# Kernel optimization log

Hardware: AMD Instinct MI355X
Metric: run time of the kernel (lower is better)

Reference implementation:

```python
import jax, jax.numpy as jnp
import numpy as np

B, N, HID = 2, 512, 768
BIAF = 256
CLS = 14
CH = 32
SIZE_DIM = 25
N_POS = 30
HSZ = 2 * (BIAF + 1) + SIZE_DIM


def setup_inputs() -> dict:
    key = jax.random.key(0)
    ks = jax.random.split(key, 16)
    s = 0.02
    return {
        "x": jax.random.normal(ks[0], (B, N, HID), jnp.float32),
        "y": jax.random.normal(ks[1], (B, N, HID), jnp.float32),
        "z": jax.random.normal(ks[2], (B, N, N, CH), jnp.float32),
        "mlp1_w": jax.random.normal(ks[3], (BIAF, HID), jnp.float32) * s,
        "mlp1_b": jnp.zeros((BIAF,), jnp.float32),
        "mlp2_w": jax.random.normal(ks[4], (BIAF, HID), jnp.float32) * s,
        "mlp2_b": jnp.zeros((BIAF,), jnp.float32),
        "head_w": jax.random.normal(ks[5], (BIAF, HID), jnp.float32) * s,
        "head_b": jnp.zeros((BIAF,), jnp.float32),
        "tail_w": jax.random.normal(ks[6], (BIAF, HID), jnp.float32) * s,
        "tail_b": jnp.zeros((BIAF,), jnp.float32),
        "biaf_W": jax.random.normal(ks[7], (CLS, BIAF + 1, BIAF + 1), jnp.float32) * s,
        "W": jax.random.normal(ks[8], (CLS, HSZ), jnp.float32) * s,
        "size_emb": jax.random.normal(ks[9], (N_POS, SIZE_DIM), jnp.float32) * s,
    }


def reference(x, y, z, mlp1_w, mlp1_b, mlp2_w, mlp2_b, head_w, head_b,
              tail_w, tail_b, biaf_W, W, size_emb):
    # MLP branches (dropout=0 at eval; torch GELU is exact erf)
    h = jax.nn.gelu(x @ mlp1_w.T + mlp1_b, approximate=False)   # (b,m,BIAF)
    t = jax.nn.gelu(y @ mlp2_w.T + mlp2_b, approximate=False)   # (b,n,BIAF)
    ones = jnp.ones(h.shape[:-1] + (1,), h.dtype)
    h1 = jnp.concatenate([h, ones], -1)                          # (b,m,BIAF+1)
    t1 = jnp.concatenate([t, ones], -1)                          # (b,n,BIAF+1)
    # Biaffine with bias_x=bias_y=True -> (b,cls,m,n)
    o1 = jnp.einsum('bmi,kij,bnj->bkmn', h1, biaf_W, t1)

    # head/tail MLPs with LeakyReLU(0.01), then append 1-column
    head = jax.nn.leaky_relu(x @ head_w.T + head_b, 0.01)
    tail = jax.nn.leaky_relu(x @ tail_w.T + tail_b, 0.01)
    head = jnp.concatenate([head, ones], -1)                     # (b,m,BIAF+1)
    tail = jnp.concatenate([tail, ones], -1)                     # (b,n,BIAF+1)

    # einsum('bmnh,kh->bkmn', cat([head_m, tail_n, size_mn]), W) decomposed so
    # the (b,m,n,HSZ) pairwise tensor is never materialized (same math).
    d = head.shape[-1]
    Wh, Wt, Ws = W[:, :d], W[:, d:2 * d], W[:, 2 * d:]
    n = x.shape[1]
    ar = jnp.arange(n)
    ids = jnp.clip(ar[None, :] - ar[:, None], -N_POS // 2, N_POS // 2 - 1) + N_POS // 2
    se = size_emb[ids]                                           # (m,n,SIZE_DIM)
    o3 = (jnp.einsum('bmh,kh->bkm', head, Wh)[:, :, :, None]
          + jnp.einsum('bnh,kh->bkn', tail, Wt)[:, :, None, :]
          + jnp.einsum('mnh,kh->kmn', se, Ws)[None])
    return o1 + o3
```

## Files before the change

kernel.cpp:

```cpp
#include <hip/hip_runtime.h>
#include <hip/hip_bf16.h>
#include <math.h>
#include <stdint.h>

#define BDIM 2
#define NDIM 512
#define HID 768
#define BIAF 256
#define CLS 14
#define DD 257
#define NPOS 30
#define SDIM 25
#define HSZ 539
#define PK 288
#define PJ 384

typedef unsigned short ushort_t;
typedef __attribute__((ext_vector_type(8))) short short8;
typedef __attribute__((ext_vector_type(4))) float floatx4;
typedef __attribute__((ext_vector_type(4))) unsigned short ushort4_t;

#define MFMA16(a, b, c) __builtin_amdgcn_mfma_f32_16x16x32_bf16((a), (b), (c), 0, 0, 0)

__device__ inline float bf2f(ushort_t u) {
    union { unsigned int i; float f; } c; c.i = ((unsigned)u) << 16; return c.f;
}
__device__ inline ushort_t f2bf(float f) {
    __hip_bfloat16 h = __float2bfloat16(f);
    return *(ushort_t*)&h;
}

__device__ inline int xcd_swz(int bid, int nwg) {
    int q = nwg >> 3;
    return (bid & 7) * q + (bid >> 3);
}

__device__ inline void glds16(const ushort_t* g, const ushort_t* l) {
    __builtin_amdgcn_global_load_lds(
        (const __attribute__((address_space(1))) unsigned int*)(unsigned long long)(uintptr_t)g,
        (__attribute__((address_space(3))) unsigned int*)(unsigned int)(uintptr_t)l,
        16, 0, 0);
}


__global__ __launch_bounds__(256) void prep_all(
    const float* __restrict__ biafW, ushort_t* __restrict__ packW,
    const float* __restrict__ x, const float* __restrict__ y,
    const float* __restrict__ m1w, const float* __restrict__ m2w,
    const float* __restrict__ hw,  const float* __restrict__ tw,
    ushort_t* __restrict__ xhi, ushort_t* __restrict__ xlo,
    ushort_t* __restrict__ yhi, ushort_t* __restrict__ ylo,
    ushort_t* __restrict__ whi, ushort_t* __restrict__ wlo,
    ushort_t* __restrict__ h1hi, ushort_t* __restrict__ h1lo,
    ushort_t* __restrict__ t1hi, ushort_t* __restrict__ t1lo)
{
    const int bid = blockIdx.x;
    if (bid < 1512) {
        __shared__ float tile[32][33];
        const int ix = bid % 9;
        const int jy = (bid / 9) % 12;
        const int k  = bid / 108;
        const int i0 = ix * 32, j0 = jy * 32;
        const int r8 = threadIdx.x >> 5;
        const int c  = threadIdx.x & 31;
        #pragma unroll
        for (int rr = 0; rr < 4; ++rr) {
            int r = rr * 8 + r8;
            int gi = i0 + r, gj = j0 + c;
            tile[r][c] = (gi < DD && gj < DD) ? biafW[((size_t)k * DD + gi) * DD + gj] : 0.f;
        }
        __syncthreads();
        #pragma unroll
        for (int rr = 0; rr < 4; ++rr) {
            int jr = rr * 8 + r8;
            packW[((size_t)k * PJ + (j0 + jr)) * PK + i0 + c] = f2bf(tile[c][jr]);
        }
        return;
    }
    int tg = (bid - 1512) * 256 + threadIdx.x;
    if (tg < 196608) {
        int mat = tg / 49152;
        int e0  = (tg % 49152) * 4;
        const float* src = (mat == 0) ? m1w : (mat == 1) ? m2w : (mat == 2) ? hw : tw;
        float4 v = *(const float4*)(src + e0);
        size_t o = (size_t)mat * 196608 + e0;
        ushort4_t h, lo;
        h[0] = f2bf(v.x); lo[0] = f2bf(v.x - bf2f(h[0]));
        h[1] = f2bf(v.y); lo[1] = f2bf(v.y - bf2f(h[1]));
        h[2] = f2bf(v.z); lo[2] = f2bf(v.z - bf2f(h[2]));
        h[3] = f2bf(v.w); lo[3] = f2bf(v.w - bf2f(h[3]));
        *(ushort4_t*)(whi + o) = h;
        *(ushort4_t*)(wlo + o) = lo;
    } else if (tg < 589824) {
        int t = tg - 196608;
        int which = t / 196608;
        int e0 = (t % 196608) * 4;
        const float* src = which ? y : x;
        float4 v = *(const float4*)(src + e0);
        ushort4_t h, lo;
        h[0] = f2bf(v.x); lo[0] = f2bf(v.x - bf2f(h[0]));
        h[1] = f2bf(v.y); lo[1] = f2bf(v.y - bf2f(h[1]));
        h[2] = f2bf(v.z); lo[2] = f2bf(v.z - bf2f(h[2]));
        h[3] = f2bf(v.w); lo[3] = f2bf(v.w - bf2f(h[3]));
        *(ushort4_t*)((which ? yhi : xhi) + e0) = h;
        *(ushort4_t*)((which ? ylo : xlo) + e0) = lo;
    } else {
        int idx = tg - 589824;
        int plane = idx >> 15;
        int tok = (idx >> 5) & 1023;
        int c   = 256 + (idx & 31);
        ushort_t* dst = (plane == 0) ? h1hi : (plane == 1) ? h1lo : (plane == 2) ? t1hi : t1lo;
        ushort_t val = (c == 256 && (plane == 0 || plane == 2)) ? (ushort_t)0x3F80 : (ushort_t)0;
        dst[(size_t)tok * PK + c] = val;
    }
}

__global__ __launch_bounds__(256) void proj_mfma(
    const ushort_t* __restrict__ xhi, const ushort_t* __restrict__ xlo,
    const ushort_t* __restrict__ yhi, const ushort_t* __restrict__ ylo,
    const ushort_t* __restrict__ whi, const ushort_t* __restrict__ wlo,
    const float* __restrict__ m1b, const float* __restrict__ m2b,
    const float* __restrict__ hb,  const float* __restrict__ tb,
    ushort_t* __restrict__ h1hi, ushort_t* __restrict__ h1lo,
    ushort_t* __restrict__ t1hi, ushort_t* __restrict__ t1lo,
    float* __restrict__ headf, float* __restrict__ tailf)
{
    const int flat = xcd_swz(blockIdx.x, 512);
    const int ft = flat & 7;
    const int mt = (flat >> 3) & 15;
    const int proj = flat >> 7;
    const int wave = threadIdx.x >> 6, L = threadIdx.x & 63;
    const int quad = L >> 4, l16 = L & 15;
    const int tok0 = mt * 64 + wave * 16;
    const int f0 = ft * 32;

    const ushort_t* ahi_p = (proj == 1) ? yhi : xhi;
    const ushort_t* alo_p = (proj == 1) ? ylo : xlo;
    const float* bias = (proj == 0) ? m1b : (proj == 1) ? m2b : (proj == 2) ? hb : tb;

    const size_t aoff = (size_t)(tok0 + l16) * HID + quad * 8;
    const size_t wbase = (size_t)proj * BIAF * HID;
    const size_t b0 = wbase + (size_t)(f0 + l16) * HID + quad * 8;
    const size_t b1 = wbase + (size_t)(f0 + 16 + l16) * HID + quad * 8;

    floatx4 acc0 = {0.f, 0.f, 0.f, 0.f}, acc1 = {0.f, 0.f, 0.f, 0.f};
    #pragma unroll 4
    for (int k0 = 0; k0 < HID; k0 += 32) {
        short8 ah  = *(const short8*)(ahi_p + aoff + k0);
        short8 al  = *(const short8*)(alo_p + aoff + k0);
        short8 bh0 = *(const short8*)(whi + b0 + k0);
        short8 bl0 = *(const short8*)(wlo + b0 + k0);
        short8 bh1 = *(const short8*)(whi + b1 + k0);
        short8 bl1 = *(const short8*)(wlo + b1 + k0);
        acc0 = MFMA16(ah, bh0, acc0);
        acc1 = MFMA16(ah, bh1, acc1);
        acc0 = MFMA16(al, bh0, acc0);
        acc1 = MFMA16(al, bh1, acc1);
        acc0 = MFMA16(ah, bl0, acc0);
        acc1 = MFMA16(ah, bl1, acc1);
    }

    #pragma unroll
    for (int nf = 0; nf < 2; ++nf) {
        floatx4 a = nf ? acc1 : acc0;
        int feat = f0 + nf * 16 + l16;
        float bv = bias[feat];
        #pragma unroll
        for (int r = 0; r < 4; ++r) {
            int tok = tok0 + quad * 4 + r;
            float v = a[r] + bv;
            if (proj <= 1) {
                float g = 0.5f * v * (1.0f + erff(v * 0.70710678118654752f));
                ushort_t h = f2bf(g);
                ushort_t lo = f2bf(g - bf2f(h));
                if (proj == 0) { h1hi[(size_t)tok * PK + feat] = h; h1lo[(size_t)tok * PK + feat] = lo; }
                else           { t1hi[(size_t)tok * PK + feat] = h; t1lo[(size_t)tok * PK + feat] = lo; }
            } else {
                float lv = (v >= 0.f) ? v : 0.01f * v;
                if (proj == 2) headf[(size_t)tok * 256 + feat] = lv;
                else           tailf[(size_t)tok * 256 + feat] = lv;
            }
        }
    }
}

__global__ __launch_bounds__(256) void mb_hk(
    const ushort_t* __restrict__ h1hi, const ushort_t* __restrict__ h1lo,
    const ushort_t* __restrict__ packW,
    ushort_t* __restrict__ Ab,
    const float* __restrict__ headf, const float* __restrict__ tailf,
    const float* __restrict__ W, const float* __restrict__ semb,
    float* __restrict__ hk, float* __restrict__ tk, float* __restrict__ skp)
{
    const int bid = blockIdx.x;
    if (bid >= 672) {
        const int hb = bid - 672;
        if (hb >= 128) {
            int idx = (hb - 128) * 256 + threadIdx.x;
            if (idx < CLS * NPOS) {
                int k = idx / NPOS, d = idx % NPOS;
                float acc = 0.f;
                for (int h = 0; h < SDIM; ++h)
                    acc += semb[d*SDIM + h] * W[k*HSZ + 2*DD + h];
                skp[idx] = acc;
            }
            return;
        }
        int p = hb * 256 + threadIdx.x;
        int which = p >> 14;
        int idx = p & 16383;
        int tok = idx >> 4;
        int k = idx & 15;
        if (k >= CLS) return;
        const float* row = (which ? tailf : headf) + (size_t)tok * 256;
        const float* wr = W + (size_t)k * HSZ + (which ? DD : 0);
        float acc = 0.f;
        for (int f4 = 0; f4 < 64; ++f4) {
            float4 rv = *(const float4*)(row + f4 * 4);
            acc += rv.x * wr[f4*4] + rv.y * wr[f4*4+1] + rv.z * wr[f4*4+2] + rv.w * wr[f4*4+3];
        }
        acc += wr[256];
        float* dst = which ? tk : hk;
        dst[(size_t)(tok >> 9) * CLS * NDIM + (size_t)k * NDIM + (tok & 511)] = acc;
        return;
    }

    __shared__ ushort_t Ah[2 * 2048];
    __shared__ ushort_t Al[2 * 2048];
    __shared__ ushort_t Bt[2 * 3072];
    const int flat = xcd_swz(bid, 672);
    const int jt = flat % 3, mt = (flat / 3) % 8, bk = flat / 24;
    const int b = bk / CLS, k = bk % CLS;
    const int tid = threadIdx.x;
    const int wave = tid >> 6, L = tid & 63;
    const int quad = L >> 4, l16 = L & 15;
    const int sr = L >> 3, u = (L & 7) ^ sr;
    const int srow = 2 * sr + (u >> 2);
    const int scol = (u & 3) * 8;
    const int rbase = (l16 >> 1) * 64 + ((((((l16 & 1) << 2) | quad)) ^ (l16 >> 1)) * 8);
    const int m0 = mt * 64, j0 = jt * 96;
    const int wm = (wave >> 1) * 32, wj = (wave & 1) * 48;

    const ushort_t* gAh = h1hi + (size_t)(b * NDIM + m0) * PK;
    const ushort_t* gAl = h1lo + (size_t)(b * NDIM + m0) * PK;
    const ushort_t* gB  = packW + ((size_t)k * PJ + j0) * PK;

    auto stage = [&](int bo, int k0) {
        for (int s = wave; s < 14; s += 4) {
            const ushort_t* g; const ushort_t* l;
            if (s < 4)      { l = Ah + bo * 2048 + s * 512;       g = gAh + (size_t)(s * 16 + srow) * PK + k0 + scol; }
            else if (s < 8) { l = Al + bo * 2048 + (s - 4) * 512; g = gAl + (size_t)((s - 4) * 16 + srow) * PK + k0 + scol; }
            else            { l = Bt + bo * 3072 + (s - 8) * 512; g = gB  + (size_t)((s - 8) * 16 + srow) * PK + k0 + scol; }
            glds16(g, l);
        }
    };

    floatx4 acc[2][3];
    #pragma unroll
    for (int mi = 0; mi < 2; ++mi)
        #pragma unroll
        for (int ni = 0; ni < 3; ++ni)
            #pragma unroll
            for (int r = 0; r < 4; ++r) acc[mi][ni][r] = 0.f;

    stage(0, 0);
    __syncthreads();
    int cur = 0;
    for (int t = 0; t < 9; ++t) {
        if (t < 8) stage(cur ^ 1, (t + 1) * 32);
        short8 ah[2], al[2], bb[3];
        #pragma unroll
        for (int mi = 0; mi < 2; ++mi) {
            ah[mi] = *(const short8*)(Ah + cur * 2048 + (wm + mi * 16) * 32 + rbase);
            al[mi] = *(const short8*)(Al + cur * 2048 + (wm + mi * 16) * 32 + rbase);
        }
        #pragma unroll
        for (int ni = 0; ni < 3; ++ni)
            bb[ni] = *(const short8*)(Bt + cur * 3072 + (wj + ni * 16) * 32 + rbase);
        #pragma unroll
        for (int mi = 0; mi < 2; ++mi)
            #pragma unroll
            for (int ni = 0; ni < 3; ++ni) {
                acc[mi][ni] = MFMA16(ah[mi], bb[ni], acc[mi][ni]);
                acc[mi][ni] = MFMA16(al[mi], bb[ni], acc[mi][ni]);
            }
        __syncthreads();
        cur ^= 1;
    }

    ushort_t* Aout = Ab + (size_t)bk * NDIM * PK;
    #pragma unroll
    for (int mi = 0; mi < 2; ++mi) {
        #pragma unroll
        for (int r = 0; r < 4; ++r) {
            int row = m0 + wm + mi * 16 + quad * 4 + r;
            #pragma unroll
            for (int ni = 0; ni < 3; ++ni) {
                int col = j0 + wj + ni * 16 + l16;
                Aout[(size_t)row * PK + col] = f2bf(acc[mi][ni][r]);
            }
        }
    }
}

__global__ __launch_bounds__(256) void mo_tile(
    const ushort_t* __restrict__ Ab,
    const ushort_t* __restrict__ t1hi, const ushort_t* __restrict__ t1lo,
    const float* __restrict__ hk, const float* __restrict__ tk,
    const float* __restrict__ sk,
    float* __restrict__ out)
{
    __shared__ ushort_t At[2 * 2048];
    __shared__ ushort_t Bh[2 * 4096];
    __shared__ ushort_t Bl[2 * 4096];
    __shared__ float skr[NPOS];
    const int flat = xcd_swz(blockIdx.x, 896);
    const int nt = flat & 3, mt = (flat >> 2) & 7, bk = flat >> 5;
    const int b = bk / CLS, k = bk % CLS;
    const int tid = threadIdx.x;
    if (tid < NPOS) skr[tid] = sk[k * NPOS + tid];
    const int wave = tid >> 6, L = tid & 63;
    const int quad = L >> 4, l16 = L & 15;
    const int sr = L >> 3, u = (L & 7) ^ sr;
    const int srow = 2 * sr + (u >> 2);
    const int scol = (u & 3) * 8;
    const int rbase = (l16 >> 1) * 64 + ((((((l16 & 1) << 2) | quad)) ^ (l16 >> 1)) * 8);
    const int m0 = mt * 64, n0 = nt * 128;
    const int wm = (wave >> 1) * 32, wn = (wave & 1) * 64;

    const ushort_t* gA  = Ab + ((size_t)bk * NDIM + m0) * PK;
    const ushort_t* gBh = t1hi + (size_t)(b * NDIM + n0) * PK;
    const ushort_t* gBl = t1lo + (size_t)(b * NDIM + n0) * PK;

    auto stage = [&](int bo, int k0) {
        for (int s = wave; s < 20; s += 4) {
            const ushort_t* g; const ushort_t* l;
            if (s < 4)       { l = At + bo * 2048 + s * 512;         g = gA  + (size_t)(s * 16 + srow) * PK + k0 + scol; }
            else if (s < 12) { l = Bh + bo * 4096 + (s - 4) * 512;   g = gBh + (size_t)((s - 4) * 16 + srow) * PK + k0 + scol; }
            else             { l = Bl + bo * 4096 + (s - 12) * 512;  g = gBl + (size_t)((s - 12) * 16 + srow) * PK + k0 + scol; }
            glds16(g, l);
        }
    };

    floatx4 acc[2][4];
    #pragma unroll
    for (int mi = 0; mi < 2; ++mi)
        #pragma unroll
        for (int ni = 0; ni < 4; ++ni)
            #pragma unroll
            for (int r = 0; r < 4; ++r) acc[mi][ni][r] = 0.f;

    stage(0, 0);
    __syncthreads();
    int cur = 0;
    for (int t = 0; t < 9; ++t) {
        if (t < 8) stage(cur ^ 1, (t + 1) * 32);
        short8 a[2], bh[4], bl[4];
        #pragma unroll
        for (int mi = 0; mi < 2; ++mi)
            a[mi] = *(const short8*)(At + cur * 2048 + (wm + mi * 16) * 32 + rbase);
        #pragma unroll
        for (int ni = 0; ni < 4; ++ni) {
            bh[ni] = *(const short8*)(Bh + cur * 4096 + (wn + ni * 16) * 32 + rbase);
            bl[ni] = *(const short8*)(Bl + cur * 4096 + (wn + ni * 16) * 32 + rbase);
        }
        #pragma unroll
        for (int mi = 0; mi < 2; ++mi)
            #pragma unroll
            for (int ni = 0; ni < 4; ++ni) {
                acc[mi][ni] = MFMA16(a[mi], bh[ni], acc[mi][ni]);
                acc[mi][ni] = MFMA16(a[mi], bl[ni], acc[mi][ni]);
            }
        __syncthreads();
        cur ^= 1;
    }

    const size_t obase = (size_t)bk * NDIM;
    #pragma unroll
    for (int mi = 0; mi < 2; ++mi) {
        #pragma unroll
        for (int r = 0; r < 4; ++r) {
            int row = m0 + wm + mi * 16 + quad * 4 + r;
            float hv = hk[obase + row];
            #pragma unroll
            for (int ni = 0; ni < 4; ++ni) {
                int col = n0 + wn + ni * 16 + l16;
                int d = col - row; d = d < -15 ? -15 : (d > 14 ? 14 : d); d += 15;
                out[(obase + row) * NDIM + col] = acc[mi][ni][r] + hv + tk[obase + col] + skr[d];
            }
        }
    }
}

extern "C" void kernel_launch(void* const* d_in, const int* in_sizes, int n_in,
                              void* d_out, int out_size, void* d_ws, size_t ws_size,
                              hipStream_t stream) {
    const float* x    = (const float*)d_in[0];
    const float* y    = (const float*)d_in[1];
    const float* m1w  = (const float*)d_in[3];
    const float* m1b  = (const float*)d_in[4];
    const float* m2w  = (const float*)d_in[5];
    const float* m2b  = (const float*)d_in[6];
    const float* hw   = (const float*)d_in[7];
    const float* hb   = (const float*)d_in[8];
    const float* tw   = (const float*)d_in[9];
    const float* tb   = (const float*)d_in[10];
    const float* biafW= (const float*)d_in[11];
    const float* W    = (const float*)d_in[12];
    const float* semb = (const float*)d_in[13];

    char* p = (char*)d_ws;
    float* hk   = (float*)p;                    p += 57344;
    float* tk   = (float*)p;                    p += 57344;
    float* skp  = (float*)p;                    p += 2048;
    float* headf= (float*)p;                    p += 1048576;
    float* tailf= (float*)p;                    p += 1048576;
    ushort_t* h1hi = (ushort_t*)p;              p += 589824;
    ushort_t* h1lo = (ushort_t*)p;              p += 589824;
    ushort_t* t1hi = (ushort_t*)p;              p += 589824;
    ushort_t* t1lo = (ushort_t*)p;              p += 589824;
    ushort_t* packW= (ushort_t*)p;              p += 3096576;
    ushort_t* whi  = (ushort_t*)p;              p += 1572864;
    ushort_t* wlo  = (ushort_t*)p;              p += 1572864;
    ushort_t* Abuf = (ushort_t*)p;              p += 8257536;
    ushort_t* xhi  = (ushort_t*)p;              p += 1572864;
    ushort_t* xlo  = (ushort_t*)p;              p += 1572864;
    ushort_t* yhi  = (ushort_t*)p;              p += 1572864;
    ushort_t* ylo  = (ushort_t*)p;              p += 1572864;

    prep_all<<<4328, 256, 0, stream>>>(biafW, packW, x, y, m1w, m2w, hw, tw,
                                       xhi, xlo, yhi, ylo, whi, wlo,
                                       h1hi, h1lo, t1hi, t1lo);
    proj_mfma<<<512, 256, 0, stream>>>(xhi, xlo, yhi, ylo, whi, wlo,
                                       m1b, m2b, hb, tb,
                                       h1hi, h1lo, t1hi, t1lo, headf, tailf);
    mb_hk<<<802, 256, 0, stream>>>(h1hi, h1lo, packW, Abuf,
                                   headf, tailf, W, semb, hk, tk, skp);
    mo_tile<<<896, 256, 0, stream>>>(Abuf, t1hi, t1lo, hk, tk, skp,
                                     (float*)d_out);
}
```

Measured before the change: 198.3 us.

## Fuse both biaffine GEMM stages into one kernel with an LDS-resident intermediate slab

Merges the two biaffine GEMMs (h1·W_k, then ·t1) into one kernel. Each block computes a 32-row slab of the intermediate A in shared memory and streams t1 tiles across all 512 columns. The hk/tk/sk projections move to a separate small kernel. This removes the global round-trip of the ~8 MB intermediate buffer and one launch. In exchange the grid shrinks to 448 blocks with serial work per block, and the first stage loses double buffering.

```diff
diff --git a/kernel.cpp b/kernel.cpp
--- a/kernel.cpp
+++ b/kernel.cpp
@@ -14,6 +14,7 @@
 #define HSZ 539
 #define PK 288
 #define PJ 384
+#define ASTRIDE 296
 
 typedef unsigned short ushort_t;
 typedef __attribute__((ext_vector_type(8))) short short8;
@@ -184,138 +185,54 @@
     }
 }
 
-__global__ __launch_bounds__(256) void mb_hk(
-    const ushort_t* __restrict__ h1hi, const ushort_t* __restrict__ h1lo,
-    const ushort_t* __restrict__ packW,
-    ushort_t* __restrict__ Ab,
+__global__ __launch_bounds__(256) void hk_tk_sk(
     const float* __restrict__ headf, const float* __restrict__ tailf,
     const float* __restrict__ W, const float* __restrict__ semb,
     float* __restrict__ hk, float* __restrict__ tk, float* __restrict__ skp)
 {
-    const int bid = blockIdx.x;
-    if (bid >= 672) {
-        const int hb = bid - 672;
-        if (hb >= 128) {
-            int idx = (hb - 128) * 256 + threadIdx.x;
-            if (idx < CLS * NPOS) {
-                int k = idx / NPOS, d = idx % NPOS;
-                float acc = 0.f;
-                for (int h = 0; h < SDIM; ++h)
-                    acc += semb[d*SDIM + h] * W[k*HSZ + 2*DD + h];
-                skp[idx] = acc;
-            }
-            return;
-        }
-        int p = hb * 256 + threadIdx.x;
-        int which = p >> 14;
-        int idx = p & 16383;
-        int tok = idx >> 4;
-        int k = idx & 15;
-        if (k >= CLS) return;
-        const float* row = (which ? tailf : headf) + (size_t)tok * 256;
-        const float* wr = W + (size_t)k * HSZ + (which ? DD : 0);
-        float acc = 0.f;
-        for (int f4 = 0; f4 < 64; ++f4) {
-            float4 rv = *(const float4*)(row + f4 * 4);
-            acc += rv.x * wr[f4*4] + rv.y * wr[f4*4+1] + rv.z * wr[f4*4+2] + rv.w * wr[f4*4+3];
-        }
-        acc += wr[256];
-        float* dst = which ? tk : hk;
-        dst[(size_t)(tok >> 9) * CLS * NDIM + (size_t)k * NDIM + (tok & 511)] = acc;
+    if (blockIdx.x >= 128) {
+        int idx = (blockIdx.x - 128) * 256 + threadIdx.x;
+        if (idx < CLS * NPOS) {
+            int k = idx / NPOS, d = idx % NPOS;
+            float acc = 0.f;
+            for (int h = 0; h < SDIM; ++h)
+                acc += semb[d*SDIM + h] * W[k*HSZ + 2*DD + h];
+            skp[idx] = acc;
+        }
         return;
     }
-
-    __shared__ ushort_t Ah[2 * 2048];
-    __shared__ ushort_t Al[2 * 2048];
-    __shared__ ushort_t Bt[2 * 3072];
-    const int flat = xcd_swz(bid, 672);
-    const int jt = flat % 3, mt = (flat / 3) % 8, bk = flat / 24;
-    const int b = bk / CLS, k = bk % CLS;
-    const int tid = threadIdx.x;
-    const int wave = tid >> 6, L = tid & 63;
-    const int quad = L >> 4, l16 = L & 15;
-    const int sr = L >> 3, u = (L & 7) ^ sr;
-    const int srow = 2 * sr + (u >> 2);
-    const int scol = (u & 3) * 8;
-    const int rbase = (l16 >> 1) * 64 + ((((((l16 & 1) << 2) | quad)) ^ (l16 >> 1)) * 8);
-    const int m0 = mt * 64, j0 = jt * 96;
-    const int wm = (wave >> 1) * 32, wj = (wave & 1) * 48;
-
-    const ushort_t* gAh = h1hi + (size_t)(b * NDIM + m0) * PK;
-    const ushort_t* gAl = h1lo + (size_t)(b * NDIM + m0) * PK;
-    const ushort_t* gB  = packW + ((size_t)k * PJ + j0) * PK;
-
-    auto stage = [&](int bo, int k0) {
-        for (int s = wave; s < 14; s += 4) {
-            const ushort_t* g; const ushort_t* l;
-            if (s < 4)      { l = Ah + bo * 2048 + s * 512;       g = gAh + (size_t)(s * 16 + srow) * PK + k0 + scol; }
-            else if (s < 8) { l = Al + bo * 2048 + (s - 4) * 512; g = gAl + (size_t)((s - 4) * 16 + srow) * PK + k0 + scol; }
-            else            { l = Bt + bo * 3072 + (s - 8) * 512; g = gB  + (size_t)((s - 8) * 16 + srow) * PK + k0 + scol; }
-            glds16(g, l);
-        }
-    };
-
-    floatx4 acc[2][3];
-    #pragma unroll
-    for (int mi = 0; mi < 2; ++mi)
-        #pragma unroll
-        for (int ni = 0; ni < 3; ++ni)
-            #pragma unroll
-            for (int r = 0; r < 4; ++r) acc[mi][ni][r] = 0.f;
-
-    stage(0, 0);
-    __syncthreads();
-    int cur = 0;
-    for (int t = 0; t < 9; ++t) {
-        if (t < 8) stage(cur ^ 1, (t + 1) * 32);
-        short8 ah[2], al[2], bb[3];
-        #pragma unroll
-        for (int mi = 0; mi < 2; ++mi) {
-            ah[mi] = *(const short8*)(Ah + cur * 2048 + (wm + mi * 16) * 32 + rbase);
-            al[mi] = *(const short8*)(Al + cur * 2048 + (wm + mi * 16) * 32 + rbase);
-        }
-        #pragma unroll
-        for (int ni = 0; ni < 3; ++ni)
-            bb[ni] = *(const short8*)(Bt + cur * 3072 + (wj + ni * 16) * 32 + rbase);
-        #pragma unroll
-        for (int mi = 0; mi < 2; ++mi)
-            #pragma unroll
-            for (int ni = 0; ni < 3; ++ni) {
-                acc[mi][ni] = MFMA16(ah[mi], bb[ni], acc[mi][ni]);
-                acc[mi][ni] = MFMA16(al[mi], bb[ni], acc[mi][ni]);
-            }
-        __syncthreads();
-        cur ^= 1;
-    }
-
-    ushort_t* Aout = Ab + (size_t)bk * NDIM * PK;
-    #pragma unroll
-    for (int mi = 0; mi < 2; ++mi) {
-        #pragma unroll
-        for (int r = 0; r < 4; ++r) {
-            int row = m0 + wm + mi * 16 + quad * 4 + r;
-            #pragma unroll
-            for (int ni = 0; ni < 3; ++ni) {
-                int col = j0 + wj + ni * 16 + l16;
-                Aout[(size_t)row * PK + col] = f2bf(acc[mi][ni][r]);
-            }
-        }
-    }
-}
-
-__global__ __launch_bounds__(256) void mo_tile(
-    const ushort_t* __restrict__ Ab,
+    int p = blockIdx.x * 256 + threadIdx.x;
+    int which = p >> 14;
+    int idx = p & 16383;
+    int tok = idx >> 4;
+    int k = idx & 15;
+    if (k >= CLS) return;
+    const float* row = (which ? tailf : headf) + (size_t)tok * 256;
+    const float* wr = W + (size_t)k * HSZ + (which ? DD : 0);
+    float acc = 0.f;
+    for (int f4 = 0; f4 < 64; ++f4) {
+        float4 rv = *(const float4*)(row + f4 * 4);
+        acc += rv.x * wr[f4*4] + rv.y * wr[f4*4+1] + rv.z * wr[f4*4+2] + rv.w * wr[f4*4+3];
+    }
+    acc += wr[256];
+    float* dst = which ? tk : hk;
+    dst[(size_t)(tok >> 9) * CLS * NDIM + (size_t)k * NDIM + (tok & 511)] = acc;
+}
+
+__global__ __launch_bounds__(256) void biaf_fused(
+    const ushort_t* __restrict__ h1hi, const ushort_t* __restrict__ h1lo,
+    const ushort_t* __restrict__ packW,
     const ushort_t* __restrict__ t1hi, const ushort_t* __restrict__ t1lo,
     const float* __restrict__ hk, const float* __restrict__ tk,
     const float* __restrict__ sk,
     float* __restrict__ out)
 {
-    __shared__ ushort_t At[2 * 2048];
-    __shared__ ushort_t Bh[2 * 4096];
-    __shared__ ushort_t Bl[2 * 4096];
+    __shared__ __align__(16) ushort_t stage[16384];
+    __shared__ __align__(16) ushort_t Aslab[32 * ASTRIDE];
     __shared__ float skr[NPOS];
-    const int flat = xcd_swz(blockIdx.x, 896);
-    const int nt = flat & 3, mt = (flat >> 2) & 7, bk = flat >> 5;
+
+    const int flat = xcd_swz(blockIdx.x, 448);
+    const int mt = flat & 15, bk = flat >> 4;
     const int b = bk / CLS, k = bk % CLS;
     const int tid = threadIdx.x;
     if (tid < NPOS) skr[tid] = sk[k * NPOS + tid];
@@ -324,69 +241,103 @@
     const int sr = L >> 3, u = (L & 7) ^ sr;
     const int srow = 2 * sr + (u >> 2);
     const int scol = (u & 3) * 8;
-    const int rbase = (l16 >> 1) * 64 + ((((((l16 & 1) << 2) | quad)) ^ (l16 >> 1)) * 8);
-    const int m0 = mt * 64, n0 = nt * 128;
-    const int wm = (wave >> 1) * 32, wn = (wave & 1) * 64;
-
-    const ushort_t* gA  = Ab + ((size_t)bk * NDIM + m0) * PK;
-    const ushort_t* gBh = t1hi + (size_t)(b * NDIM + n0) * PK;
-    const ushort_t* gBl = t1lo + (size_t)(b * NDIM + n0) * PK;
-
-    auto stage = [&](int bo, int k0) {
-        for (int s = wave; s < 20; s += 4) {
+    const int rbase = (l16 >> 1) * 64 + (((((l16 & 1) << 2) | quad) ^ (l16 >> 1)) * 8);
+    const int m0 = mt * 32;
+
+    const ushort_t* gAh = h1hi + (size_t)(b * NDIM + m0) * PK;
+    const ushort_t* gAl = h1lo + (size_t)(b * NDIM + m0) * PK;
+    const ushort_t* gB  = packW + (size_t)k * PJ * PK;
+
+    const int mi = wave >> 1, jh = wave & 1;
+    floatx4 accA[9];
+    #pragma unroll
+    for (int t = 0; t < 9; ++t)
+        #pragma unroll
+        for (int r = 0; r < 4; ++r) accA[t][r] = 0.f;
+
+    for (int i0 = 0; i0 < PK; i0 += 32) {
+        for (int s = wave; s < 22; s += 4) {
             const ushort_t* g; const ushort_t* l;
-            if (s < 4)       { l = At + bo * 2048 + s * 512;         g = gA  + (size_t)(s * 16 + srow) * PK + k0 + scol; }
-            else if (s < 12) { l = Bh + bo * 4096 + (s - 4) * 512;   g = gBh + (size_t)((s - 4) * 16 + srow) * PK + k0 + scol; }
-            else             { l = Bl + bo * 4096 + (s - 12) * 512;  g = gBl + (size_t)((s - 12) * 16 + srow) * PK + k0 + scol; }
+            if (s < 2)      { l = stage + s * 512;  g = gAh + (size_t)(s * 16 + srow) * PK + i0 + scol; }
+            else if (s < 4) { l = stage + s * 512;  g = gAl + (size_t)((s - 2) * 16 + srow) * PK + i0 + scol; }
+            else            { l = stage + s * 512;  g = gB  + (size_t)((s - 4) * 16 + srow) * PK + i0 + scol; }
             glds16(g, l);
         }
+        __syncthreads();
+        short8 ah = *(const short8*)(stage + mi * 512 + rbase);
+        short8 al = *(const short8*)(stage + 1024 + mi * 512 + rbase);
+        #pragma unroll
+        for (int t = 0; t < 9; ++t) {
+            short8 bt = *(const short8*)(stage + 2048 + (jh * 9 + t) * 512 + rbase);
+            accA[t] = MFMA16(ah, bt, accA[t]);
+            accA[t] = MFMA16(al, bt, accA[t]);
+        }
+        __syncthreads();
+    }
+
+    #pragma unroll
+    for (int t = 0; t < 9; ++t) {
+        int jb = (jh * 9 + t) * 16 + l16;
+        #pragma unroll
+        for (int r = 0; r < 4; ++r) {
+            int row = mi * 16 + quad * 4 + r;
+            Aslab[row * ASTRIDE + jb] = f2bf(accA[t][r]);
+        }
+    }
+    __syncthreads();
+
+    const int mi2 = wave >> 1, nh = wave & 1;
+    const ushort_t* gTh = t1hi + (size_t)(b * NDIM) * PK;
+    const ushort_t* gTl = t1lo + (size_t)(b * NDIM) * PK;
+
+    auto stageB = [&](int bo, int nt, int js) {
+        for (int s = wave; s < 16; s += 4) {
+            const ushort_t* g; const ushort_t* l;
+            if (s < 8) { l = stage + bo * 8192 + s * 512;
+                         g = gTh + (size_t)(nt * 128 + s * 16 + srow) * PK + js * 32 + scol; }
+            else       { l = stage + bo * 8192 + 4096 + (s - 8) * 512;
+                         g = gTl + (size_t)(nt * 128 + (s - 8) * 16 + srow) * PK + js * 32 + scol; }
+            glds16(g, l);
+        }
     };
 
-    floatx4 acc[2][4];
-    #pragma unroll
-    for (int mi = 0; mi < 2; ++mi)
-        #pragma unroll
-        for (int ni = 0; ni < 4; ++ni)
-            #pragma unroll
-            for (int r = 0; r < 4; ++r) acc[mi][ni][r] = 0.f;
-
-    stage(0, 0);
+    stageB(0, 0, 0);
     __syncthreads();
     int cur = 0;
-    for (int t = 0; t < 9; ++t) {
-        if (t < 8) stage(cur ^ 1, (t + 1) * 32);
-        short8 a[2], bh[4], bl[4];
-        #pragma unroll
-        for (int mi = 0; mi < 2; ++mi)
-            a[mi] = *(const short8*)(At + cur * 2048 + (wm + mi * 16) * 32 + rbase);
-        #pragma unroll
-        for (int ni = 0; ni < 4; ++ni) {
-            bh[ni] = *(const short8*)(Bh + cur * 4096 + (wn + ni * 16) * 32 + rbase);
-            bl[ni] = *(const short8*)(Bl + cur * 4096 + (wn + ni * 16) * 32 + rbase);
-        }
-        #pragma unroll
-        for (int mi = 0; mi < 2; ++mi)
+    const size_t obase = (size_t)bk * NDIM;
+
+    for (int nt = 0; nt < 4; ++nt) {
+        floatx4 accB[4];
+        #pragma unroll
+        for (int nf = 0; nf < 4; ++nf)
             #pragma unroll
-            for (int ni = 0; ni < 4; ++ni) {
-                acc[mi][ni] = MFMA16(a[mi], bh[ni], acc[mi][ni]);
-                acc[mi][ni] = MFMA16(a[mi], bl[ni], acc[mi][ni]);
+            for (int r = 0; r < 4; ++r) accB[nf][r] = 0.f;
+
+        for (int js = 0; js < 9; ++js) {
+            int step = nt * 9 + js;
+            if (step < 35) { int ns = step + 1; stageB(cur ^ 1, ns / 9, ns % 9); }
+            short8 a = *(const short8*)(Aslab + (mi2 * 16 + l16) * ASTRIDE + js * 32 + quad * 8);
+            #pragma unroll
+            for (int nf = 0; nf < 4; ++nf) {
+                short8 bh = *(const short8*)(stage + cur * 8192 + (nh * 4 + nf) * 512 + rbase);
+                short8 bl = *(const short8*)(stage + cur * 8192 + 4096 + (nh * 4 + nf) * 512 + rbase);
+                accB[nf] = MFMA16(a, bh, accB[nf]);
+                accB[nf] = MFMA16(a, bl, accB[nf]);
             }
-        __syncthreads();
-        cur ^= 1;
-    }
-
-    const size_t obase = (size_t)bk * NDIM;
-    #pragma unroll
-    for (int mi = 0; mi < 2; ++mi) {
+            __syncthreads();
+            cur ^= 1;
+        }
+
+        int n0 = nt * 128;
         #pragma unroll
         for (int r = 0; r < 4; ++r) {
-            int row = m0 + wm + mi * 16 + quad * 4 + r;
+            int row = m0 + mi2 * 16 + quad * 4 + r;
             float hv = hk[obase + row];
             #pragma unroll
-            for (int ni = 0; ni < 4; ++ni) {
-                int col = n0 + wn + ni * 16 + l16;
+            for (int nf = 0; nf < 4; ++nf) {
+                int col = n0 + nh * 64 + nf * 16 + l16;
                 int d = col - row; d = d < -15 ? -15 : (d > 14 ? 14 : d); d += 15;
-                out[(obase + row) * NDIM + col] = acc[mi][ni][r] + hv + tk[obase + col] + skr[d];
+                out[(obase + row) * NDIM + col] = accB[nf][r] + hv + tk[obase + col] + skr[d];
             }
         }
     }
@@ -422,7 +373,6 @@
     ushort_t* packW= (ushort_t*)p;              p += 3096576;
     ushort_t* whi  = (ushort_t*)p;              p += 1572864;
     ushort_t* wlo  = (ushort_t*)p;              p += 1572864;
-    ushort_t* Abuf = (ushort_t*)p;              p += 8257536;
     ushort_t* xhi  = (ushort_t*)p;              p += 1572864;
     ushort_t* xlo  = (ushort_t*)p;              p += 1572864;
     ushort_t* yhi  = (ushort_t*)p;              p += 1572864;
@@ -434,8 +384,7 @@
     proj_mfma<<<512, 256, 0, stream>>>(xhi, xlo, yhi, ylo, whi, wlo,
                                        m1b, m2b, hb, tb,
                                        h1hi, h1lo, t1hi, t1lo, headf, tailf);
-    mb_hk<<<802, 256, 0, stream>>>(h1hi, h1lo, packW, Abuf,
-                                   headf, tailf, W, semb, hk, tk, skp);
-    mo_tile<<<896, 256, 0, stream>>>(Abuf, t1hi, t1lo, hk, tk, skp,
-                                     (float*)d_out);
-}
+    hk_tk_sk<<<130, 256, 0, stream>>>(headf, tailf, W, semb, hk, tk, skp);
+    biaf_fused<<<448, 256, 0, stream>>>(h1hi, h1lo, packW, t1hi, t1lo,
+                                        hk, tk, skp, (float*)d_out);
+}
```

After: 207.5 us. 1.05x slower.

## Stage projection GEMM tiles through double-buffered swizzled LDS with direct global-to-LDS loads

Applied to the files above, without the earlier changes.

The projection kernel used to load A and W fragments straight from global memory into registers for each MFMA step. It now copies 32-wide K slices of the A (hi/lo) and W (hi/lo) tiles into a double-buffered shared-memory area using a global-to-LDS helper. The next slice is prefetched while MFMAs run on the current one. An XOR swizzle is meant to avoid LDS bank conflicts, and W tiles are shared across the four waves. The cost is one block barrier per K step plus LDS occupancy.

```diff
diff --git a/kernel.cpp b/kernel.cpp
--- a/kernel.cpp
+++ b/kernel.cpp
@@ -125,12 +125,17 @@
     ushort_t* __restrict__ t1hi, ushort_t* __restrict__ t1lo,
     float* __restrict__ headf, float* __restrict__ tailf)
 {
+    __shared__ __align__(16) ushort_t Sh[2 * 6144];
     const int flat = xcd_swz(blockIdx.x, 512);
     const int ft = flat & 7;
     const int mt = (flat >> 3) & 15;
     const int proj = flat >> 7;
     const int wave = threadIdx.x >> 6, L = threadIdx.x & 63;
     const int quad = L >> 4, l16 = L & 15;
+    const int sr = L >> 3, u = (L & 7) ^ sr;
+    const int srow = 2 * sr + (u >> 2);
+    const int scol = (u & 3) * 8;
+    const int rbase = (l16 >> 1) * 64 + (((((l16 & 1) << 2) | quad) ^ (l16 >> 1)) * 8);
     const int tok0 = mt * 64 + wave * 16;
     const int f0 = ft * 32;
 
@@ -138,26 +143,44 @@
     const ushort_t* alo_p = (proj == 1) ? ylo : xlo;
     const float* bias = (proj == 0) ? m1b : (proj == 1) ? m2b : (proj == 2) ? hb : tb;
 
-    const size_t aoff = (size_t)(tok0 + l16) * HID + quad * 8;
+    const ushort_t* gAh = ahi_p + (size_t)(mt * 64) * HID;
+    const ushort_t* gAl = alo_p + (size_t)(mt * 64) * HID;
     const size_t wbase = (size_t)proj * BIAF * HID;
-    const size_t b0 = wbase + (size_t)(f0 + l16) * HID + quad * 8;
-    const size_t b1 = wbase + (size_t)(f0 + 16 + l16) * HID + quad * 8;
+    const ushort_t* gWh = whi + wbase + (size_t)f0 * HID;
+    const ushort_t* gWl = wlo + wbase + (size_t)f0 * HID;
+
+    auto stage = [&](int bo, int k0) {
+        for (int s = wave; s < 12; s += 4) {
+            const ushort_t* g;
+            if (s < 4)       g = gAh + (size_t)(s * 16 + srow) * HID + k0 + scol;
+            else if (s < 8)  g = gAl + (size_t)((s - 4) * 16 + srow) * HID + k0 + scol;
+            else if (s < 10) g = gWh + (size_t)((s - 8) * 16 + srow) * HID + k0 + scol;
+            else             g = gWl + (size_t)((s - 10) * 16 + srow) * HID + k0 + scol;
+            glds16(g, Sh + bo * 6144 + s * 512);
+        }
+    };
 
     floatx4 acc0 = {0.f, 0.f, 0.f, 0.f}, acc1 = {0.f, 0.f, 0.f, 0.f};
-    #pragma unroll 4
-    for (int k0 = 0; k0 < HID; k0 += 32) {
-        short8 ah  = *(const short8*)(ahi_p + aoff + k0);
-        short8 al  = *(const short8*)(alo_p + aoff + k0);
-        short8 bh0 = *(const short8*)(whi + b0 + k0);
-        short8 bl0 = *(const short8*)(wlo + b0 + k0);
-        short8 bh1 = *(const short8*)(whi + b1 + k0);
-        short8 bl1 = *(const short8*)(wlo + b1 + k0);
+    stage(0, 0);
+    __syncthreads();
+    int cur = 0;
+    for (int t = 0; t < 24; ++t) {
+        if (t < 23) stage(cur ^ 1, (t + 1) * 32);
+        const ushort_t* B = Sh + cur * 6144;
+        short8 ah  = *(const short8*)(B + wave * 512 + rbase);
+        short8 al  = *(const short8*)(B + 2048 + wave * 512 + rbase);
+        short8 bh0 = *(const short8*)(B + 4096 + rbase);
+        short8 bh1 = *(const short8*)(B + 4608 + rbase);
+        short8 bl0 = *(const short8*)(B + 5120 + rbase);
+        short8 bl1 = *(const short8*)(B + 5632 + rbase);
         acc0 = MFMA16(ah, bh0, acc0);
         acc1 = MFMA16(ah, bh1, acc1);
         acc0 = MFMA16(al, bh0, acc0);
         acc1 = MFMA16(al, bh1, acc1);
         acc0 = MFMA16(ah, bl0, acc0);
         acc1 = MFMA16(ah, bl1, acc1);
+        __syncthreads();
+        cur ^= 1;
     }
 
     #pragma unroll
```

After: 180.1 us. 1.1x faster.
